# Kernel tuning notes

Hardware: AMD Instinct MI355X
Metric: run time of the kernel (lower is better)

## Reference

```python
import jax, jax.numpy as jnp
import numpy as np

CANVAS_SHAPE = (4096, 4096)
WIDTH = 20.0
ANTI_ALIASING_FACTOR = 1.0
EPSILON = 0.001


def setup_inputs() -> dict:
    key = jax.random.key(0)
    # key_points: list of one normalized [y, x] point in [0, 1); modeled as [1, 2]
    key_points = jax.random.uniform(key, (1, 2), dtype=jnp.float32)
    return {"key_points": key_points}


def reference(key_points) -> jnp.ndarray:
    H, W = CANVAS_SHAPE
    shape_vec = jnp.asarray(CANVAS_SHAPE, dtype=jnp.float32)  # [2]
    # scale normalized point into pixel coordinates (matches key_point * canvas_shape_tensor)
    p = key_points[0] * shape_vec  # [2] -> (py, px)
    # torch.norm(canvas_shape - [0,0])
    max_distance = jnp.sqrt(jnp.sum(shape_vec * shape_vec))
    ys = jnp.arange(H, dtype=jnp.float32)[:, None]  # [H, 1]
    xs = jnp.arange(W, dtype=jnp.float32)[None, :]  # [1, W]
    # per-pixel Euclidean distance to the point, fully vectorized
    dist = jnp.sqrt((ys - p[0]) ** 2 + (xs - p[1]) ** 2)  # [H, W]
    val = 1.0 - (dist / max_distance + EPSILON) ** ANTI_ALIASING_FACTOR
    canvas = jnp.where(dist < WIDTH, val, 0.0)
    return canvas
```

## Files before the change

kernel.cpp:

```cpp
#include <hip/hip_runtime.h>


__global__ __launch_bounds__(256) void point_graphic2d_kernel(
    const float* __restrict__ key_points, float* __restrict__ out) {
  constexpr int H = 4096;
  constexpr int W = 4096;
  constexpr float WIDTH = 20.0f;
  constexpr float EPS = 0.001f;
  constexpr float INV_MAXD = 1.0f / 5792.61880957152f;

  const float py = key_points[0] * (float)H;
  const float px = key_points[1] * (float)W;

  constexpr int N4 = (H * W) / 4;
  const int stride = gridDim.x * blockDim.x;

  for (int i = blockIdx.x * blockDim.x + threadIdx.x; i < N4; i += stride) {
    const int y  = i >> 10;
    const int x0 = (i & 1023) << 2;

    float vv[4] = {0.0f, 0.0f, 0.0f, 0.0f};

    const float dy = (float)y - py;
    if (fabsf(dy) < WIDTH) {
      const float fx0 = (float)x0;
      if (fx0 + 3.0f > px - WIDTH && fx0 < px + WIDTH) {
        const float dy2 = dy * dy;
#pragma unroll
        for (int j = 0; j < 4; ++j) {
          const float dx = fx0 + (float)j - px;
          const float dist = sqrtf(dy2 + dx * dx);
          if (dist < WIDTH) {
            vv[j] = 1.0f - (dist * INV_MAXD + EPS);
          }
        }
      }
    }

    float4 v;
    v.x = vv[0]; v.y = vv[1]; v.z = vv[2]; v.w = vv[3];
    reinterpret_cast<float4*>(out)[i] = v;
  }
}

extern "C" void kernel_launch(void* const* d_in, const int* in_sizes, int n_in,
                              void* d_out, int out_size, void* d_ws, size_t ws_size,
                              hipStream_t stream) {
  const float* key_points = (const float*)d_in[0];
  float* out = (float*)d_out;

  dim3 grid(2048);
  dim3 block(256);
  hipLaunchKernelGGL(point_graphic2d_kernel, grid, block, 0, stream,
                     key_points, out);
}
```

Before: 16.52 us.

## Zero canvas with memset and compute only a small window around the point

Replaces the full-canvas grid-stride kernel with a hipMemsetAsync zero fill followed by a tiny kernel that only evaluates pixels in a 64x48 window near the point. It aims to skip per-pixel arithmetic and branching over the whole canvas. The output write volume is unchanged, so the cost is still dominated by writing 64 MB, and the change adds a second launch on the stream.

```diff
diff --git a/kernel.cpp b/kernel.cpp
--- a/kernel.cpp
+++ b/kernel.cpp
@@ -1,7 +1,7 @@
 #include <hip/hip_runtime.h>
 
 
-__global__ __launch_bounds__(256) void point_graphic2d_kernel(
+__global__ __launch_bounds__(256) void disk_kernel(
     const float* __restrict__ key_points, float* __restrict__ out) {
   constexpr int H = 4096;
   constexpr int W = 4096;
@@ -12,34 +12,18 @@
   const float py = key_points[0] * (float)H;
   const float px = key_points[1] * (float)W;
 
-  constexpr int N4 = (H * W) / 4;
-  const int stride = gridDim.x * blockDim.x;
+  const int y0 = max(0, (int)ceilf(py - WIDTH));
+  const int x0 = max(0, (int)ceilf(px - WIDTH));
 
-  for (int i = blockIdx.x * blockDim.x + threadIdx.x; i < N4; i += stride) {
-    const int y  = i >> 10;
-    const int x0 = (i & 1023) << 2;
+  const int x = x0 + (int)threadIdx.x;
+  const int y = y0 + (int)(blockIdx.y * blockDim.y + threadIdx.y);
+  if (x >= W || y >= H) return;
 
-    float vv[4] = {0.0f, 0.0f, 0.0f, 0.0f};
-
-    const float dy = (float)y - py;
-    if (fabsf(dy) < WIDTH) {
-      const float fx0 = (float)x0;
-      if (fx0 + 3.0f > px - WIDTH && fx0 < px + WIDTH) {
-        const float dy2 = dy * dy;
-#pragma unroll
-        for (int j = 0; j < 4; ++j) {
-          const float dx = fx0 + (float)j - px;
-          const float dist = sqrtf(dy2 + dx * dx);
-          if (dist < WIDTH) {
-            vv[j] = 1.0f - (dist * INV_MAXD + EPS);
-          }
-        }
-      }
-    }
-
-    float4 v;
-    v.x = vv[0]; v.y = vv[1]; v.z = vv[2]; v.w = vv[3];
-    reinterpret_cast<float4*>(out)[i] = v;
+  const float dx = (float)x - px;
+  const float dy = (float)y - py;
+  const float dist = sqrtf(dx * dx + dy * dy);
+  if (dist < WIDTH) {
+    out[(size_t)y * W + x] = 1.0f - (dist * INV_MAXD + EPS);
   }
 }
 
@@ -49,8 +33,9 @@
   const float* key_points = (const float*)d_in[0];
   float* out = (float*)d_out;
 
-  dim3 grid(2048);
-  dim3 block(256);
-  hipLaunchKernelGGL(point_graphic2d_kernel, grid, block, 0, stream,
-                     key_points, out);
+  hipMemsetAsync(out, 0, (size_t)out_size * sizeof(float), stream);
+
+  dim3 block(64, 4);
+  dim3 grid(1, 12);
+  hipLaunchKernelGGL(disk_kernel, grid, block, 0, stream, key_points, out);
 }
```

Measured after the change: 17.06 us. +3.3%, slower.
